# Kernel tuning notes

Measured on AMD Instinct MI355X. Metric: run time of the kernel, lower is better.

The kernel has to match this reference:

```python
import jax, jax.numpy as jnp
import numpy as np

N_TOKENS = 16384
DIM = 2048
N_EXPERTS = 64
TOPK = 8
ROUTE_SCALE = 1.0


def setup_inputs() -> dict:
    key = jax.random.key(0)
    k1, k2 = jax.random.split(key)
    x = jax.random.normal(k1, (N_TOKENS, DIM), dtype=jnp.float32)
    W = jax.random.normal(k2, (N_EXPERTS, DIM), dtype=jnp.float32) * 0.02
    return {"x": x, "W": W}


def reference(x, W):
    # linear scores: [tokens, n_experts]
    logits = jnp.einsum('td,ed->te', x, W)
    # softmax in float32 (score_func == 'softmax'); bias is None since dim != 64
    scores = jax.nn.softmax(logits.astype(jnp.float32), axis=-1)
    # top-k expert selection, then gather original scores at selected indices
    _, indices = jax.lax.top_k(scores, TOPK)
    weights = jnp.take_along_axis(scores, indices, axis=-1)
    # softmax path: no renormalization, just route scaling
    weights = (weights * ROUTE_SCALE).astype(x.dtype)
    return weights, indices
```

## Files before the change

kernel.cpp:

```cpp
#include <hip/hip_runtime.h>


typedef __attribute__((ext_vector_type(8))) short short8;
typedef __attribute__((ext_vector_type(4))) float f32x4;

#define NT    16384
#define DIMK  2048
#define NE    64
#define TOPKK 8
#define TT    32
#define CH    32
#define WS_BYTES (CH * 24 * 1024)

union U4S8 { unsigned int u[4]; short8 s; };

__device__ __forceinline__ void split3(const float4 a, const float4 b,
                                       short8& H, short8& M, short8& L) {
    const float f[8] = {a.x, a.y, a.z, a.w, b.x, b.y, b.z, b.w};
    U4S8 uh, um, ul;
#pragma unroll
    for (int p = 0; p < 4; ++p) {
        const float f0 = f[2 * p], f1 = f[2 * p + 1];
        const unsigned int t0 = __float_as_uint(f0) & 0xFFFF0000u;
        const unsigned int t1 = __float_as_uint(f1) & 0xFFFF0000u;
        uh.u[p] = (t0 >> 16) | t1;
        const float r0 = f0 - __uint_as_float(t0);
        const float r1 = f1 - __uint_as_float(t1);
        const unsigned int v0 = __float_as_uint(r0) & 0xFFFF0000u;
        const unsigned int v1 = __float_as_uint(r1) & 0xFFFF0000u;
        um.u[p] = (v0 >> 16) | v1;
        const float s0 = r0 - __uint_as_float(v0);
        const float s1 = r1 - __uint_as_float(v1);
        ul.u[p] = (__float_as_uint(s0) >> 16) | (__float_as_uint(s1) & 0xFFFF0000u);
    }
    H = uh.s; M = um.s; L = ul.s;
}

__device__ __forceinline__ f32x4 mfma6(short8 ah, short8 am, short8 al,
                                       short8 bh, short8 bm, short8 bl, f32x4 c) {
    c = __builtin_amdgcn_mfma_f32_16x16x32_bf16(ah, bh, c, 0, 0, 0);
    c = __builtin_amdgcn_mfma_f32_16x16x32_bf16(ah, bm, c, 0, 0, 0);
    c = __builtin_amdgcn_mfma_f32_16x16x32_bf16(am, bh, c, 0, 0, 0);
    c = __builtin_amdgcn_mfma_f32_16x16x32_bf16(ah, bl, c, 0, 0, 0);
    c = __builtin_amdgcn_mfma_f32_16x16x32_bf16(am, bm, c, 0, 0, 0);
    c = __builtin_amdgcn_mfma_f32_16x16x32_bf16(al, bh, c, 0, 0, 0);
    return c;
}

__device__ __forceinline__ void async16(void* lds, const void* gp) {
    __builtin_amdgcn_global_load_lds(
        (const __attribute__((address_space(1))) unsigned int*)gp,
        (__attribute__((address_space(3))) unsigned int*)lds, 16, 0, 0);
}

#define SCHED_FENCE() __builtin_amdgcn_sched_barrier(0)
#define VM_WAIT8() do { asm volatile("s_waitcnt vmcnt(8)" ::: "memory"); SCHED_FENCE(); } while (0)
#define VM_WAIT0() do { asm volatile("s_waitcnt vmcnt(0)" ::: "memory"); SCHED_FENCE(); } while (0)
#define BAR() do { SCHED_FENCE(); __builtin_amdgcn_s_barrier(); SCHED_FENCE(); } while (0)

__global__ __launch_bounds__(64) void pack_w_kernel(
    const float* __restrict__ W, short* __restrict__ wp)
{
    const int b = blockIdx.x;
    const int c = b >> 3, sp = (b >> 2) & 1, n = b & 3;
    const int l = threadIdx.x;
    const float* g = W + (size_t)(16 * n + (l & 15)) * DIMK
                       + 64 * c + 32 * sp + 8 * (l >> 4);
    const float4 lo = *(const float4*)g;
    const float4 hi = *(const float4*)(g + 4);
    short8 H, M, L;
    split3(lo, hi, H, M, L);
    const size_t base = ((size_t)c * 24 + (sp * 4 + n) * 3) * 512 + l * 8;
    *(short8*)(wp + base)        = H;
    *(short8*)(wp + base + 512)  = M;
    *(short8*)(wp + base + 1024) = L;
}

__global__ __launch_bounds__(256, 2) void gate_main_kernel(
    const float* __restrict__ x, const short* __restrict__ wp,
    float* __restrict__ out)
{
    __shared__ __align__(16) char smem[65536];

    const int tid = threadIdx.x;
    const int w   = tid >> 6;
    const int l   = tid & 63;
    const int lj  = l & 15;
    const int lq  = l >> 4;
    const int tg  = w >> 1;
    const int eg  = w & 1;
    const int bt0 = blockIdx.x * TT;

#define STAGE(cc, B) do {                                                     \
    _Pragma("unroll")                                                         \
    for (int ii = 0; ii < 2; ++ii) {                                          \
        const int i = 2 * w + ii;                                             \
        const int r = 4 * i + lq;                                             \
        const float* gsrc = x + (size_t)(bt0 + r) * DIMK + (cc) * 64          \
                              + ((lj ^ (r & 7)) << 2);                        \
        async16(smem + (B) * 8192 + i * 1024, gsrc);                          \
    }                                                                         \
    _Pragma("unroll")                                                         \
    for (int ii = 0; ii < 6; ++ii) {                                          \
        const int f = 6 * w + ii;                                             \
        const short* gs = wp + ((size_t)(cc) * 24 + f) * 512 + l * 8;         \
        async16(smem + 16384 + (B) * 24576 + f * 1024, gs);                   \
    }                                                                         \
} while (0)

#define COMPUTE(B) do {                                                       \
    const float4* xv = (const float4*)(smem + (B) * 8192);                    \
    const short8* wv = (const short8*)(smem + 16384 + (B) * 24576);           \
    _Pragma("unroll")                                                         \
    for (int sp = 0; sp < 2; ++sp) {                                          \
        const int row = 16 * tg + lj;                                         \
        const int rx  = row & 7;                                              \
        const float4 a0 = xv[row * 16 + ((8 * sp + 2 * lq + 0) ^ rx)];        \
        const float4 a1 = xv[row * 16 + ((8 * sp + 2 * lq + 1) ^ rx)];        \
        short8 ah, am, al_;                                                   \
        split3(a0, a1, ah, am, al_);                                          \
        _Pragma("unroll")                                                     \
        for (int nt = 0; nt < 2; ++nt) {                                      \
            const int n  = 2 * eg + nt;                                       \
            const int fb = (sp * 4 + n) * 3;                                  \
            const short8 bh = wv[(fb + 0) * 64 + l];                          \
            const short8 bm = wv[(fb + 1) * 64 + l];                          \
            const short8 bl = wv[(fb + 2) * 64 + l];                          \
            acc[nt] = mfma6(ah, am, al_, bh, bm, bl, acc[nt]);                \
        }                                                                     \
    }                                                                         \
} while (0)

    f32x4 acc[2];
#pragma unroll
    for (int nt = 0; nt < 2; ++nt) acc[nt] = (f32x4){0.f, 0.f, 0.f, 0.f};

    STAGE(0, 0);
    STAGE(1, 1);

#pragma unroll 1
    for (int c = 0; c < CH; c += 2) {
        VM_WAIT8();
        BAR();
        COMPUTE(0);
        BAR();
        if (c + 2 < CH) { STAGE(c + 2, 0); VM_WAIT8(); }
        else            { VM_WAIT0(); }
        BAR();
        COMPUTE(1);
        BAR();
        if (c + 3 < CH) STAGE(c + 3, 1);
    }

    float* lg = (float*)smem;
#pragma unroll
    for (int nt = 0; nt < 2; ++nt)
#pragma unroll
        for (int q = 0; q < 4; ++q)
            lg[(16 * tg + 4 * lq + q) * (NE + 1) + 32 * eg + 16 * nt + lj] =
                acc[nt][q];
    __syncthreads();

    if (tid < TT) {
        const float* rowp = lg + tid * (NE + 1);
        float mx = -3.402823466e38f;
        for (int e = 0; e < NE; ++e) mx = fmaxf(mx, rowp[e]);
        float sden = 0.f;
        for (int e = 0; e < NE; ++e) sden += expf(rowp[e] - mx);

        float tv[TOPKK];
        int   ti[TOPKK];
#pragma unroll
        for (int i = 0; i < TOPKK; ++i) { tv[i] = -3.402823466e38f; ti[i] = 0; }
        for (int e = 0; e < NE; ++e) {
            const float v = rowp[e];
            if (v > tv[TOPKK - 1]) {
                tv[TOPKK - 1] = v; ti[TOPKK - 1] = e;
#pragma unroll
                for (int q = TOPKK - 1; q > 0; --q) {
                    if (tv[q] > tv[q - 1]) {
                        const float fv = tv[q]; tv[q] = tv[q - 1]; tv[q - 1] = fv;
                        const int   iv = ti[q]; ti[q] = ti[q - 1]; ti[q - 1] = iv;
                    }
                }
            }
        }
        float* ow = out + (size_t)(bt0 + tid) * TOPKK;
        float* oi = out + (size_t)NT * TOPKK + (size_t)(bt0 + tid) * TOPKK;
#pragma unroll
        for (int i = 0; i < TOPKK; ++i) {
            ow[i] = expf(tv[i] - mx) / sden;
            oi[i] = (float)ti[i];
        }
    }
#undef STAGE
#undef COMPUTE
}

__device__ __forceinline__ void load_step(const float* xp0, const float* xp1,
                                          const float* wp, int koff,
                                          float4 xb[2][2], float4 wb[4][2]) {
#pragma unroll
    for (int h = 0; h < 2; ++h) {
        xb[0][h] = *(const float4*)(xp0 + koff + 4 * h);
        xb[1][h] = *(const float4*)(xp1 + koff + 4 * h);
    }
#pragma unroll
    for (int n = 0; n < 4; ++n)
#pragma unroll
        for (int h = 0; h < 2; ++h)
            wb[n][h] = *(const float4*)(wp + (size_t)n * 16 * DIMK + koff + 4 * h);
}

__device__ __forceinline__ void do_step(const float4 xc[2][2], const float4 wc[4][2],
                                        f32x4 acc[2][4]) {
    short8 ah[2], am[2], al[2];
#pragma unroll
    for (int m = 0; m < 2; ++m) split3(xc[m][0], xc[m][1], ah[m], am[m], al[m]);
#pragma unroll
    for (int n = 0; n < 4; ++n) {
        short8 bh, bm, bl;
        split3(wc[n][0], wc[n][1], bh, bm, bl);
#pragma unroll
        for (int m = 0; m < 2; ++m)
            acc[m][n] = mfma6(ah[m], am[m], al[m], bh, bm, bl, acc[m][n]);
    }
}

__global__ __launch_bounds__(256, 2) void gate_fallback_kernel(
    const float* __restrict__ x, const float* __restrict__ W,
    float* __restrict__ out)
{
    __shared__ float lg[4][32][NE + 1];
    const int tid = threadIdx.x;
    const int w = tid >> 6, l = tid & 63;
    const int j = l & 15, g = l >> 4;
    const int bt0 = blockIdx.x * 32;
    const int kb = w * 512;
    const float* xp0 = x + (size_t)(bt0 + j) * DIMK + kb + 8 * g;
    const float* xp1 = xp0 + (size_t)16 * DIMK;
    const float* wpp = W + (size_t)j * DIMK + kb + 8 * g;
    f32x4 acc[2][4];
#pragma unroll
    for (int m = 0; m < 2; ++m)
#pragma unroll
        for (int n = 0; n < 4; ++n) acc[m][n] = (f32x4){0.f, 0.f, 0.f, 0.f};
    float4 xA[2][2], wA[4][2], xB[2][2], wB[4][2];
    load_step(xp0, xp1, wpp, 0, xA, wA);
#pragma unroll 1
    for (int s = 0; s < 16; s += 2) {
        load_step(xp0, xp1, wpp, 32 * (s + 1), xB, wB);
        do_step(xA, wA, acc);
        if (s + 2 < 16) load_step(xp0, xp1, wpp, 32 * (s + 2), xA, wA);
        do_step(xB, wB, acc);
    }
#pragma unroll
    for (int m = 0; m < 2; ++m)
#pragma unroll
        for (int n = 0; n < 4; ++n)
#pragma unroll
            for (int q = 0; q < 4; ++q)
                lg[w][16 * m + 4 * g + q][16 * n + j] = acc[m][n][q];
    __syncthreads();
#pragma unroll
    for (int r = 0; r < 8; ++r) {
        const int idx = tid + r * 256;
        const int t = idx >> 6, e = idx & 63;
        lg[0][t][e] += lg[1][t][e] + lg[2][t][e] + lg[3][t][e];
    }
    __syncthreads();
    if (tid < 32) {
        const float* rowp = &lg[0][tid][0];
        float mx = -3.402823466e38f;
        for (int e = 0; e < NE; ++e) mx = fmaxf(mx, rowp[e]);
        float sden = 0.f;
        for (int e = 0; e < NE; ++e) sden += expf(rowp[e] - mx);
        float tv[TOPKK]; int ti[TOPKK];
#pragma unroll
        for (int i = 0; i < TOPKK; ++i) { tv[i] = -3.402823466e38f; ti[i] = 0; }
        for (int e = 0; e < NE; ++e) {
            const float v = rowp[e];
            if (v > tv[TOPKK - 1]) {
                tv[TOPKK - 1] = v; ti[TOPKK - 1] = e;
#pragma unroll
                for (int q = TOPKK - 1; q > 0; --q)
                    if (tv[q] > tv[q - 1]) {
                        const float fv = tv[q]; tv[q] = tv[q - 1]; tv[q - 1] = fv;
                        const int iv = ti[q]; ti[q] = ti[q - 1]; ti[q - 1] = iv;
                    }
            }
        }
        float* ow = out + (size_t)(bt0 + tid) * TOPKK;
        float* oi = out + (size_t)NT * TOPKK + (size_t)(bt0 + tid) * TOPKK;
#pragma unroll
        for (int i = 0; i < TOPKK; ++i) {
            ow[i] = expf(tv[i] - mx) / sden;
            oi[i] = (float)ti[i];
        }
    }
}

extern "C" void kernel_launch(void* const* d_in, const int* in_sizes, int n_in,
                              void* d_out, int out_size, void* d_ws, size_t ws_size,
                              hipStream_t stream) {
    const float* x = (const float*)d_in[0];
    const float* W = (const float*)d_in[1];
    float* out = (float*)d_out;
    if (ws_size >= (size_t)WS_BYTES) {
        short* wp = (short*)d_ws;
        hipLaunchKernelGGL(pack_w_kernel, dim3(256), dim3(64), 0, stream, W, wp);
        hipLaunchKernelGGL(gate_main_kernel, dim3(NT / TT), dim3(256), 0, stream,
                           x, wp, out);
    } else {
        hipLaunchKernelGGL(gate_fallback_kernel, dim3(NT / 32), dim3(256), 0, stream,
                           x, W, out);
    }
}
```

Baseline: 64.19 us.

## Switch gate GEMM to 32x32 MFMA with 64-token tiles and triple buffering

Doubles the token tile to 64 with 512-thread blocks and switches from 16x16x32 to 32x32x16 bf16 MFMA, so each wave computes a 32x32 output tile over half of each K chunk. The two K halves are reduced through LDS afterwards. The pipeline moves from double to triple buffering (120KB dynamic LDS) with adjusted waitcnt values, and the W packing layout changes to match the 32-wide B fragments. The aim is fewer LDS reads per FLOP and better latency hiding. In exchange it drops to one block per CU and adds a cross-wave reduction step.

Result: no change. 65.38 us (+1.9%).

```diff
diff --git a/kernel.cpp b/kernel.cpp
--- a/kernel.cpp
+++ b/kernel.cpp
@@ -2,14 +2,16 @@
 
 
 typedef __attribute__((ext_vector_type(8))) short short8;
+typedef __attribute__((ext_vector_type(16))) float f32x16;
 typedef __attribute__((ext_vector_type(4))) float f32x4;
 
 #define NT    16384
 #define DIMK  2048
 #define NE    64
 #define TOPKK 8
-#define TT    32
+#define TT    64
 #define CH    32
+#define BUFB  40960
 #define WS_BYTES (CH * 24 * 1024)
 
 union U4S8 { unsigned int u[4]; short8 s; };
@@ -36,14 +38,15 @@
     H = uh.s; M = um.s; L = ul.s;
 }
 
-__device__ __forceinline__ f32x4 mfma6(short8 ah, short8 am, short8 al,
-                                       short8 bh, short8 bm, short8 bl, f32x4 c) {
-    c = __builtin_amdgcn_mfma_f32_16x16x32_bf16(ah, bh, c, 0, 0, 0);
-    c = __builtin_amdgcn_mfma_f32_16x16x32_bf16(ah, bm, c, 0, 0, 0);
-    c = __builtin_amdgcn_mfma_f32_16x16x32_bf16(am, bh, c, 0, 0, 0);
-    c = __builtin_amdgcn_mfma_f32_16x16x32_bf16(ah, bl, c, 0, 0, 0);
-    c = __builtin_amdgcn_mfma_f32_16x16x32_bf16(am, bm, c, 0, 0, 0);
-    c = __builtin_amdgcn_mfma_f32_16x16x32_bf16(al, bh, c, 0, 0, 0);
+__device__ __forceinline__ f32x16 mfma6w(short8 ah, short8 am, short8 al,
+                                         short8 bh, short8 bm, short8 bl,
+                                         f32x16 c) {
+    c = __builtin_amdgcn_mfma_f32_32x32x16_bf16(ah, bh, c, 0, 0, 0);
+    c = __builtin_amdgcn_mfma_f32_32x32x16_bf16(ah, bm, c, 0, 0, 0);
+    c = __builtin_amdgcn_mfma_f32_32x32x16_bf16(am, bh, c, 0, 0, 0);
+    c = __builtin_amdgcn_mfma_f32_32x32x16_bf16(ah, bl, c, 0, 0, 0);
+    c = __builtin_amdgcn_mfma_f32_32x32x16_bf16(am, bm, c, 0, 0, 0);
+    c = __builtin_amdgcn_mfma_f32_32x32x16_bf16(al, bh, c, 0, 0, 0);
     return c;
 }
 
@@ -54,42 +57,50 @@
 }
 
 #define SCHED_FENCE() __builtin_amdgcn_sched_barrier(0)
-#define VM_WAIT8() do { asm volatile("s_waitcnt vmcnt(8)" ::: "memory"); SCHED_FENCE(); } while (0)
-#define VM_WAIT0() do { asm volatile("s_waitcnt vmcnt(0)" ::: "memory"); SCHED_FENCE(); } while (0)
+#define VM_WAIT10() do { asm volatile("s_waitcnt vmcnt(10)" ::: "memory"); SCHED_FENCE(); } while (0)
+#define VM_WAIT5()  do { asm volatile("s_waitcnt vmcnt(5)"  ::: "memory"); SCHED_FENCE(); } while (0)
+#define VM_WAIT0()  do { asm volatile("s_waitcnt vmcnt(0)"  ::: "memory"); SCHED_FENCE(); } while (0)
 #define BAR() do { SCHED_FENCE(); __builtin_amdgcn_s_barrier(); SCHED_FENCE(); } while (0)
 
 __global__ __launch_bounds__(64) void pack_w_kernel(
-    const float* __restrict__ W, short* __restrict__ wp)
+    const float* __restrict__ W, short* __restrict__ wpk)
 {
-    const int b = blockIdx.x;
-    const int c = b >> 3, sp = (b >> 2) & 1, n = b & 3;
-    const int l = threadIdx.x;
-    const float* g = W + (size_t)(16 * n + (l & 15)) * DIMK
-                       + 64 * c + 32 * sp + 8 * (l >> 4);
+    const int b  = blockIdx.x;
+    const int c  = b >> 3, fg = b & 7;
+    const int s  = fg >> 1, n32 = fg & 1;
+    const int l  = threadIdx.x;
+    const float* g = W + (size_t)(32 * n32 + (l & 31)) * DIMK
+                       + 64 * c + 16 * s + 8 * (l >> 5);
     const float4 lo = *(const float4*)g;
     const float4 hi = *(const float4*)(g + 4);
     short8 H, M, L;
     split3(lo, hi, H, M, L);
-    const size_t base = ((size_t)c * 24 + (sp * 4 + n) * 3) * 512 + l * 8;
-    *(short8*)(wp + base)        = H;
-    *(short8*)(wp + base + 512)  = M;
-    *(short8*)(wp + base + 1024) = L;
-}
-
-__global__ __launch_bounds__(256, 2) void gate_main_kernel(
+    const size_t base = ((size_t)(c * 8 + fg) * 3) * 512 + l * 8;
+    *(short8*)(wpk + base)        = H;
+    *(short8*)(wpk + base + 512)  = M;
+    *(short8*)(wpk + base + 1024) = L;
+}
+
+__global__ __launch_bounds__(512, 1) void gate_main_kernel(
     const float* __restrict__ x, const short* __restrict__ wp,
     float* __restrict__ out)
 {
-    __shared__ __align__(16) char smem[65536];
+    extern __shared__ __align__(16) char smem[];
 
     const int tid = threadIdx.x;
     const int w   = tid >> 6;
     const int l   = tid & 63;
     const int lj  = l & 15;
     const int lq  = l >> 4;
-    const int tg  = w >> 1;
-    const int eg  = w & 1;
+    const int l5  = l >> 5;
+    const int r31 = l & 31;
+    const int tg  = (w >> 2) & 1;
+    const int eg  = (w >> 1) & 1;
+    const int sph = w & 1;
     const int bt0 = blockIdx.x * TT;
+
+#define XB(B) (smem + (B) * BUFB)
+#define WBUF(B) (smem + (B) * BUFB + 16384)
 
 #define STAGE(cc, B) do {                                                     \
     _Pragma("unroll")                                                         \
@@ -98,67 +109,84 @@
         const int r = 4 * i + lq;                                             \
         const float* gsrc = x + (size_t)(bt0 + r) * DIMK + (cc) * 64          \
                               + ((lj ^ (r & 7)) << 2);                        \
-        async16(smem + (B) * 8192 + i * 1024, gsrc);                          \
+        async16(XB(B) + i * 1024, gsrc);                                      \
     }                                                                         \
     _Pragma("unroll")                                                         \
-    for (int ii = 0; ii < 6; ++ii) {                                          \
-        const int f = 6 * w + ii;                                             \
-        const short* gs = wp + ((size_t)(cc) * 24 + f) * 512 + l * 8;         \
-        async16(smem + 16384 + (B) * 24576 + f * 1024, gs);                   \
+    for (int t = 0; t < 3; ++t) {                                             \
+        const int F = 3 * w + t;                                              \
+        const short* gs = wp + ((size_t)(cc) * 24 + F) * 512 + l * 8;         \
+        async16(WBUF(B) + F * 1024, gs);                                      \
     }                                                                         \
 } while (0)
 
 #define COMPUTE(B) do {                                                       \
-    const float4* xv = (const float4*)(smem + (B) * 8192);                    \
-    const short8* wv = (const short8*)(smem + 16384 + (B) * 24576);           \
+    const char* xb = XB(B);                                                   \
+    const char* wb = WBUF(B);                                                 \
+    const int row = 32 * tg + r31;                                            \
+    const int rx  = row & 7;                                                  \
     _Pragma("unroll")                                                         \
-    for (int sp = 0; sp < 2; ++sp) {                                          \
-        const int row = 16 * tg + lj;                                         \
-        const int rx  = row & 7;                                              \
-        const float4 a0 = xv[row * 16 + ((8 * sp + 2 * lq + 0) ^ rx)];        \
-        const float4 a1 = xv[row * 16 + ((8 * sp + 2 * lq + 1) ^ rx)];        \
-        short8 ah, am, al_;                                                   \
-        split3(a0, a1, ah, am, al_);                                          \
-        _Pragma("unroll")                                                     \
-        for (int nt = 0; nt < 2; ++nt) {                                      \
-            const int n  = 2 * eg + nt;                                       \
-            const int fb = (sp * 4 + n) * 3;                                  \
-            const short8 bh = wv[(fb + 0) * 64 + l];                          \
-            const short8 bm = wv[(fb + 1) * 64 + l];                          \
-            const short8 bl = wv[(fb + 2) * 64 + l];                          \
-            acc[nt] = mfma6(ah, am, al_, bh, bm, bl, acc[nt]);                \
-        }                                                                     \
+    for (int ks = 0; ks < 2; ++ks) {                                          \
+        const int s   = 2 * sph + ks;                                         \
+        const int sl0 = (4 * s + 2 * l5 + 0) ^ rx;                            \
+        const int sl1 = (4 * s + 2 * l5 + 1) ^ rx;                            \
+        const float4 a0 = *(const float4*)(xb + row * 256 + sl0 * 16);        \
+        const float4 a1 = *(const float4*)(xb + row * 256 + sl1 * 16);        \
+        short8 H, M, L;                                                       \
+        split3(a0, a1, H, M, L);                                              \
+        const int F = (2 * s + eg) * 3;                                       \
+        const short8 bh  = *(const short8*)(wb + (F + 0) * 1024 + l * 16);    \
+        const short8 bm  = *(const short8*)(wb + (F + 1) * 1024 + l * 16);    \
+        const short8 bl_ = *(const short8*)(wb + (F + 2) * 1024 + l * 16);    \
+        acc = mfma6w(H, M, L, bh, bm, bl_, acc);                              \
     }                                                                         \
 } while (0)
 
-    f32x4 acc[2];
-#pragma unroll
-    for (int nt = 0; nt < 2; ++nt) acc[nt] = (f32x4){0.f, 0.f, 0.f, 0.f};
+    f32x16 acc;
+#pragma unroll
+    for (int i = 0; i < 16; ++i) acc[i] = 0.f;
 
     STAGE(0, 0);
     STAGE(1, 1);
+    STAGE(2, 2);
 
 #pragma unroll 1
-    for (int c = 0; c < CH; c += 2) {
-        VM_WAIT8();
-        BAR();
+    for (int cb = 0; cb < CH - 2; cb += 3) {
+        VM_WAIT10(); BAR();
         COMPUTE(0);
         BAR();
-        if (c + 2 < CH) { STAGE(c + 2, 0); VM_WAIT8(); }
-        else            { VM_WAIT0(); }
-        BAR();
+        STAGE(cb + 3, 0);
+
+        VM_WAIT10(); BAR();
         COMPUTE(1);
         BAR();
-        if (c + 3 < CH) STAGE(c + 3, 1);
-    }
+        STAGE(cb + 4, 1);
+
+        VM_WAIT10(); BAR();
+        COMPUTE(2);
+        BAR();
+        if (cb + 5 < CH) STAGE(cb + 5, 2);
+    }
+    VM_WAIT5(); BAR();
+    COMPUTE(0);
+    BAR();
+    VM_WAIT0(); BAR();
+    COMPUTE(1);
+    BAR();
 
     float* lg = (float*)smem;
 #pragma unroll
-    for (int nt = 0; nt < 2; ++nt)
-#pragma unroll
-        for (int q = 0; q < 4; ++q)
-            lg[(16 * tg + 4 * lq + q) * (NE + 1) + 32 * eg + 16 * nt + lj] =
-                acc[nt][q];
+    for (int r = 0; r < 16; ++r) {
+        const int rowc = (r & 3) + 8 * (r >> 2) + 4 * l5;
+        lg[(sph * TT + 32 * tg + rowc) * (NE + 1) + 32 * eg + r31] = acc[r];
+    }
+    __syncthreads();
+
+#pragma unroll
+    for (int rr = 0; rr < (TT * NE) / 512; ++rr) {
+        const int idx = tid + rr * 512;
+        const int t = idx >> 6, e = idx & 63;
+        lg[t * (NE + 1) + e] += lg[(TT + t) * (NE + 1) + e];
+    }
     __syncthreads();
 
     if (tid < TT) {
@@ -195,6 +223,19 @@
     }
 #undef STAGE
 #undef COMPUTE
+#undef XB
+#undef WBUF
+}
+
+__device__ __forceinline__ f32x4 mfma6s(short8 ah, short8 am, short8 al,
+                                        short8 bh, short8 bm, short8 bl, f32x4 c) {
+    c = __builtin_amdgcn_mfma_f32_16x16x32_bf16(ah, bh, c, 0, 0, 0);
+    c = __builtin_amdgcn_mfma_f32_16x16x32_bf16(ah, bm, c, 0, 0, 0);
+    c = __builtin_amdgcn_mfma_f32_16x16x32_bf16(am, bh, c, 0, 0, 0);
+    c = __builtin_amdgcn_mfma_f32_16x16x32_bf16(ah, bl, c, 0, 0, 0);
+    c = __builtin_amdgcn_mfma_f32_16x16x32_bf16(am, bm, c, 0, 0, 0);
+    c = __builtin_amdgcn_mfma_f32_16x16x32_bf16(al, bh, c, 0, 0, 0);
+    return c;
 }
 
 __device__ __forceinline__ void load_step(const float* xp0, const float* xp1,
@@ -223,7 +264,7 @@
         split3(wc[n][0], wc[n][1], bh, bm, bl);
 #pragma unroll
         for (int m = 0; m < 2; ++m)
-            acc[m][n] = mfma6(ah[m], am[m], al[m], bh, bm, bl, acc[m][n]);
+            acc[m][n] = mfma6s(ah[m], am[m], al[m], bh, bm, bl, acc[m][n]);
     }
 }
 
@@ -307,10 +348,10 @@
     const float* W = (const float*)d_in[1];
     float* out = (float*)d_out;
     if (ws_size >= (size_t)WS_BYTES) {
-        short* wp = (short*)d_ws;
-        hipLaunchKernelGGL(pack_w_kernel, dim3(256), dim3(64), 0, stream, W, wp);
-        hipLaunchKernelGGL(gate_main_kernel, dim3(NT / TT), dim3(256), 0, stream,
-                           x, wp, out);
+        short* wpk = (short*)d_ws;
+        hipLaunchKernelGGL(pack_w_kernel, dim3(256), dim3(64), 0, stream, W, wpk);
+        hipLaunchKernelGGL(gate_main_kernel, dim3(NT / TT), dim3(512),
+                           3 * BUFB, stream, x, wpk, out);
     } else {
         hipLaunchKernelGGL(gate_fallback_kernel, dim3(NT / 32), dim3(256), 0, stream,
                            x, W, out);
```
